# Performance work log

Hardware: AMD Instinct MI355X
Metric: run time of the kernel (lower is better)

## Reference

```python
import jax, jax.numpy as jnp
import numpy as np

NUM_EXPERTS = 4
TOP_K = 2


def setup_inputs() -> dict:
    key = jax.random.key(0)
    ks = jax.random.split(key, 16)
    B, L, D, E, H = 8, 768, 1024, NUM_EXPERTS, 4096
    s = 0.02
    return {
        "context_c": jax.random.normal(ks[0], (B, L, D), jnp.float32),
        "time_cond": jax.random.normal(ks[1], (B, D), jnp.float32),
        "gate_w": jax.random.normal(ks[2], (3 * D, E), jnp.float32) * s,
        "gate_b": jnp.zeros((E,), jnp.float32),
        "time_w": jax.random.normal(ks[3], (D, 2 * E), jnp.float32) * s,
        "time_b": jnp.zeros((2 * E,), jnp.float32),
        "ew1": jax.random.normal(ks[4], (E, D, H), jnp.float32) * s,
        "eb1": jnp.zeros((E, H), jnp.float32),
        "ew2": jax.random.normal(ks[5], (E, H, D), jnp.float32) * s,
        "eb2": jnp.zeros((E, D), jnp.float32),
        "sw1": jax.random.normal(ks[6], (D, H), jnp.float32) * s,
        "sb1": jnp.zeros((H,), jnp.float32),
        "sw2": jax.random.normal(ks[7], (H, D), jnp.float32) * s,
        "sb2": jnp.zeros((D,), jnp.float32),
    }


def reference(context_c, time_cond, gate_w, gate_b, time_w, time_b,
              ew1, eb1, ew2, eb2, sw1, sb1, sw2, sb2):
    B, L, D = context_c.shape
    E, K = NUM_EXPERTS, TOP_K
    L_head = L_wrist = L // 3

    head = context_c[:, :L_head]                       # (B, Lh, D)
    wrist = context_c[:, L_head:L_head + L_wrist]      # (B, Lw, D)
    proprio = context_c[:, L_head + L_wrist:]          # (B, Lp, D)

    # modality-combination aggregates for the gate
    full_agg = context_c.mean(axis=1)
    hp_agg = jnp.concatenate([head, proprio], axis=1).mean(axis=1)
    wp_agg = jnp.concatenate([wrist, proprio], axis=1).mean(axis=1)
    gate_in = jnp.concatenate([full_agg, hp_agg, wp_agg], axis=-1)  # (B, 3D)

    gate_logits = gate_in @ gate_w + gate_b            # (B, E)
    mod = jax.nn.silu(time_cond) @ time_w + time_b     # (B, 2E)
    scale, shift = jnp.split(mod, 2, axis=-1)
    gate_logits = gate_logits * (1.0 + scale) + shift

    gate_scores = jax.nn.softmax(gate_logits, axis=-1)
    topk_w, topk_i = jax.lax.top_k(gate_scores, K)     # (B, K)
    topk_w = topk_w / (topk_w.sum(axis=-1, keepdims=True) + 1e-8)

    # per-sample combine weight per expert: (B, E)
    onehot = (topk_i[..., None] == jnp.arange(E)[None, None, :]).astype(context_c.dtype)
    w_be = jnp.sum(topk_w[..., None] * onehot, axis=1)

    # modality token masks per expert: expert 1 skips wrist, expert 2 skips head
    mask = np.ones((E, L), dtype=np.float32)
    mask[1, L_head:L_head + L_wrist] = 0.0
    mask[2, :L_head] = 0.0
    mask = jnp.asarray(mask)

    out = jnp.zeros_like(context_c)
    for e in range(E):  # small fixed expert loop; FFN is tokenwise so masking == routing
        h = jax.nn.gelu(context_c @ ew1[e] + eb1[e], approximate=True)
        y = h @ ew2[e] + eb2[e]                        # (B, L, D)
        out = out + (w_be[:, e][:, None, None] * mask[e][None, :, None]) * y

    shared = jax.nn.gelu(context_c @ sw1 + sb1, approximate=True) @ sw2 + sb2
    return out + shared
```

## Files before the change

kernel.cpp:

```cpp
#include <hip/hip_runtime.h>

using bf16x8 = __attribute__((ext_vector_type(8))) short;
using f32x4  = __attribute__((ext_vector_type(4))) float;
using u16x4  = __attribute__((ext_vector_type(4))) unsigned short;

#define AS1(p) ((__attribute__((address_space(1))) void*)(p))
#define AS3(p) ((__attribute__((address_space(3))) void*)(p))

__device__ __forceinline__ unsigned short f2bf(float f){
  unsigned int x = __float_as_uint(f);
  unsigned int r = (x + 0x7FFFu + ((x >> 16) & 1u)) >> 16;
  return (unsigned short)r;
}
__device__ __forceinline__ float gelu_tanh(float x){
  float u = 0.7978845608028654f * (x + 0.044715f * x * x * x);
  float t = 1.f - 2.f / (__expf(2.f * u) + 1.f);
  return 0.5f * x * (1.f + t);
}

static constexpr int BB = 8, LL = 768, DD = 1024, HH = 4096, TT = 6144;

__global__ __launch_bounds__(256) void k0_transpose(const float* __restrict__ srcE,
                                                    const float* __restrict__ srcS,
                                                    unsigned short* __restrict__ dst,
                                                    int R, int C){
  __shared__ float tile[64][65];
  int z = blockIdx.z;
  const float* src = (z < 4) ? srcE + (size_t)z * R * C : srcS;
  unsigned short* d = dst + (size_t)z * R * C;
  int c0 = blockIdx.x * 64, r0 = blockIdx.y * 64;
  int tx = threadIdx.x & 15, ty = threadIdx.x >> 4;
  #pragma unroll
  for (int rep = 0; rep < 4; rep++){
    int r = ty + rep * 16;
    float4 v = *(const float4*)(src + (size_t)(r0 + r) * C + c0 + tx * 4);
    tile[r][tx * 4 + 0] = v.x; tile[r][tx * 4 + 1] = v.y;
    tile[r][tx * 4 + 2] = v.z; tile[r][tx * 4 + 3] = v.w;
  }
  __syncthreads();
  #pragma unroll
  for (int rep = 0; rep < 4; rep++){
    int c = ty + rep * 16;
    u16x4 o;
    o[0] = f2bf(tile[tx * 4 + 0][c]); o[1] = f2bf(tile[tx * 4 + 1][c]);
    o[2] = f2bf(tile[tx * 4 + 2][c]); o[3] = f2bf(tile[tx * 4 + 3][c]);
    *(u16x4*)(d + (size_t)(c0 + c) * R + r0 + tx * 4) = o;
  }
}

__global__ __launch_bounds__(256) void k1x_cvt_partial(const float* __restrict__ X,
                                                       unsigned short* __restrict__ Xb,
                                                       float* __restrict__ part){
  int ch = blockIdx.x, b = blockIdx.y, t = threadIdx.x;
  size_t rowbase = ((size_t)(b * LL + ch * 32)) * DD;
  const float4* src = (const float4*)(X + rowbase);
  u16x4* dst = (u16x4*)(Xb + rowbase);
  float4 s; s.x = s.y = s.z = s.w = 0.f;
  for (int l = 0; l < 32; l++){
    float4 v = src[l * 256 + t];
    u16x4 o;
    o[0] = f2bf(v.x); o[1] = f2bf(v.y); o[2] = f2bf(v.z); o[3] = f2bf(v.w);
    dst[l * 256 + t] = o;
    s.x += v.x; s.y += v.y; s.z += v.z; s.w += v.w;
  }
  ((float4*)(part + ((size_t)(b * 24 + ch)) * DD))[t] = s;
}

__global__ __launch_bounds__(256) void k1b_gate(const float* __restrict__ part,
                                                const float* __restrict__ tc,
                                                const float* __restrict__ gw,
                                                const float* __restrict__ gb,
                                                const float* __restrict__ tw,
                                                const float* __restrict__ tb,
                                                float* __restrict__ wtop, int* __restrict__ itop){
  int b = blockIdx.x, t = threadIdx.x;
  __shared__ float glog[4], gmod[8];
  if (t < 4) glog[t] = 0.f;
  if (t < 8) gmod[t] = 0.f;
  __syncthreads();
  float lacc[4] = {0.f,0.f,0.f,0.f};
  float macc[8] = {0.f,0.f,0.f,0.f,0.f,0.f,0.f,0.f};
  for (int dd = 0; dd < 4; dd++){
    int d = dd * 256 + t;
    const float* pb = part + (size_t)b * 24 * DD + d;
    float sh = 0.f, sw = 0.f, sp = 0.f;
    for (int c2 = 0; c2 < 8; c2++){
      sh += pb[(0  + c2) * DD];
      sw += pb[(8  + c2) * DD];
      sp += pb[(16 + c2) * DD];
    }
    float fa = (sh + sw + sp) * (1.f / 768.f);
    float hp = (sh + sp) * (1.f / 512.f);
    float wp = (sw + sp) * (1.f / 512.f);
    #pragma unroll
    for (int e = 0; e < 4; e++){
      lacc[e] += fa * gw[(size_t)d * 4 + e]
               + hp * gw[(size_t)(DD + d) * 4 + e]
               + wp * gw[(size_t)(2 * DD + d) * 4 + e];
    }
    float v = tc[(size_t)b * DD + d];
    float sl = v / (1.f + __expf(-v));
    #pragma unroll
    for (int j = 0; j < 8; j++) macc[j] += sl * tw[(size_t)d * 8 + j];
  }
  #pragma unroll
  for (int e = 0; e < 4; e++) atomicAdd(&glog[e], lacc[e]);
  #pragma unroll
  for (int j = 0; j < 8; j++) atomicAdd(&gmod[j], macc[j]);
  __syncthreads();
  if (t == 0){
    float lg[4];
    #pragma unroll
    for (int e = 0; e < 4; e++){
      float sc = gmod[e]     + tb[e];
      float sf = gmod[4 + e] + tb[4 + e];
      lg[e] = (glog[e] + gb[e]) * (1.f + sc) + sf;
    }
    float mx = fmaxf(fmaxf(lg[0], lg[1]), fmaxf(lg[2], lg[3]));
    float p[4], s = 0.f;
    #pragma unroll
    for (int e = 0; e < 4; e++){ p[e] = __expf(lg[e] - mx); s += p[e]; }
    #pragma unroll
    for (int e = 0; e < 4; e++) p[e] /= s;
    int i0 = 0;
    for (int e = 1; e < 4; e++) if (p[e] > p[i0]) i0 = e;
    int i1 = (i0 == 0) ? 1 : 0;
    for (int e = 0; e < 4; e++) if (e != i0 && p[e] > p[i1]) i1 = e;
    float den = p[i0] + p[i1] + 1e-8f;
    wtop[b * 2 + 0] = p[i0] / den;  wtop[b * 2 + 1] = p[i1] / den;
    itop[b * 2 + 0] = i0;           itop[b * 2 + 1] = i1;
  }
}

#define MMA_Q(AF, BQ, MH, NH)                                                   \
  {                                                                             \
    _Pragma("unroll") for (int ks = 0; ks < 2; ks++)                            \
    _Pragma("unroll") for (int mf = 0; mf < 4; mf++)                            \
    _Pragma("unroll") for (int nf = 0; nf < 2; nf++)                            \
      acc[(MH)*4+mf][(NH)*2+nf] = __builtin_amdgcn_mfma_f32_16x16x32_bf16(      \
          (AF)[mf][ks], (BQ)[nf][ks], acc[(MH)*4+mf][(NH)*2+nf], 0, 0, 0);      \
  }

__device__ __forceinline__ void gemm256_core(const unsigned short* __restrict__ A,
                                             const unsigned short* __restrict__ B,
                                             int lda, int ldb, int nkt,
                                             unsigned short* ldsA,
                                             unsigned short* ldsB,
                                             f32x4 (&acc)[8][4]){
  const int t = threadIdx.x;
  const int lane = t & 63, quad = lane >> 4, r = lane & 15;
  const int wave = t >> 6, wm = wave >> 2, wn = wave & 3;
  const int welem = (t & 448) * 8;

  int offA[2], offB[2];
  #pragma unroll
  for (int j = 0; j < 2; j++){
    int x = t * 16 + j * 8192;
    int y = x ^ (((x >> 7) & 7) << 4);
    int cr = y >> 7, kel = (y & 127) >> 1;
    offA[j] = (((cr >> 6) << 7) + (cr & 63)) * lda + kel;
    offB[j] = (((cr >> 5) << 6) + (cr & 31)) * ldb + kel;
  }
  const int ldam = 64 * lda, ldbn = 32 * ldb;

  auto stA = [&](int buf, int mh, int kt){
    #pragma unroll
    for (int j = 0; j < 2; j++)
      __builtin_amdgcn_global_load_lds(AS1(A + offA[j] + mh * ldam + kt * 64),
          AS3(ldsA + (buf * 2 + mh) * 8192 + welem + j * 4096), 16, 0, 0);
  };
  auto stB = [&](int buf, int nh, int kt){
    #pragma unroll
    for (int j = 0; j < 2; j++)
      __builtin_amdgcn_global_load_lds(AS1(B + offB[j] + nh * ldbn + kt * 64),
          AS3(ldsB + (buf * 2 + nh) * 8192 + welem + j * 4096), 16, 0, 0);
  };
  auto ldA = [&](int buf, int mh, bf16x8 (&dst)[4][2]){
    #pragma unroll
    for (int mf = 0; mf < 4; mf++){
      int cr = wm * 64 + mf * 16 + r;
      const unsigned short* p = ldsA + (buf * 2 + mh) * 8192 + cr * 64;
      int sw = (cr & 7) << 3;
      dst[mf][0] = *(const bf16x8*)(p + ((quad * 8) ^ sw));
      dst[mf][1] = *(const bf16x8*)(p + ((32 + quad * 8) ^ sw));
    }
  };
  auto ldB = [&](int buf, int nh, bf16x8 (&dst)[2][2]){
    #pragma unroll
    for (int nf = 0; nf < 2; nf++){
      int cc = wn * 32 + nf * 16 + r;
      const unsigned short* p = ldsB + (buf * 2 + nh) * 8192 + cc * 64;
      int sw = (cc & 7) << 3;
      dst[nf][0] = *(const bf16x8*)(p + ((quad * 8) ^ sw));
      dst[nf][1] = *(const bf16x8*)(p + ((32 + quad * 8) ^ sw));
    }
  };

  stA(0, 0, 0); stB(0, 0, 0); stB(0, 1, 0); stA(0, 1, 0);
  stA(1, 0, 1); stB(1, 0, 1); stB(1, 1, 1);
  asm volatile("s_waitcnt vmcnt(6)" ::: "memory");
  __builtin_amdgcn_s_barrier();

  bf16x8 af[4][2], b0[2][2], b1[2][2];
  for (int kt = 0; kt < nkt; kt++){
    int buf = kt & 1;
    bool pf1 = (kt + 1 < nkt), pf2 = (kt + 2 < nkt);
    ldA(buf, 0, af); ldB(buf, 0, b0);
    if (pf1) stA(buf ^ 1, 1, kt + 1);
    __builtin_amdgcn_s_barrier();
    __builtin_amdgcn_s_setprio(1);
    MMA_Q(af, b0, 0, 0);
    __builtin_amdgcn_s_setprio(0);
    __builtin_amdgcn_s_barrier();
    ldB(buf, 1, b1);
    if (pf2) stA(buf, 0, kt + 2);
    __builtin_amdgcn_s_barrier();
    __builtin_amdgcn_s_setprio(1);
    MMA_Q(af, b1, 0, 1);
    __builtin_amdgcn_s_setprio(0);
    __builtin_amdgcn_s_barrier();
    ldA(buf, 1, af);
    if (pf2) stB(buf, 0, kt + 2);
    __builtin_amdgcn_s_barrier();
    __builtin_amdgcn_s_setprio(1);
    MMA_Q(af, b1, 1, 1);
    __builtin_amdgcn_s_setprio(0);
    __builtin_amdgcn_s_barrier();
    if (pf2) stB(buf, 1, kt + 2);
    __builtin_amdgcn_s_barrier();
    __builtin_amdgcn_s_setprio(1);
    MMA_Q(af, b0, 1, 0);
    __builtin_amdgcn_s_setprio(0);
    if (pf1){
      if (pf2) asm volatile("s_waitcnt vmcnt(6)" ::: "memory");
      else     asm volatile("s_waitcnt vmcnt(0)" ::: "memory");
    }
    __builtin_amdgcn_s_barrier();
  }
}

__device__ __forceinline__ void mask_weight(int e, int seg, float& w){
  if ((e == 1 && seg == 1) || (e == 2 && seg == 0)) w = 0.f;
}

__global__ __launch_bounds__(512, 2) void k2_gemm1(const unsigned short* __restrict__ Xb,
                                                   const unsigned short* __restrict__ w1t,
                                                   const float* __restrict__ eb1,
                                                   const float* __restrict__ sb1,
                                                   const float* __restrict__ wtop,
                                                   const int* __restrict__ itop,
                                                   unsigned short* __restrict__ Hws){
  int m0 = blockIdx.x * 256, n0 = blockIdx.y * 256, slot = blockIdx.z;
  int b = m0 / LL, seg = (m0 % LL) / 256;
  int mat; float w;
  if (slot == 0){ mat = 4; w = 1.f; }
  else {
    int k = slot - 1;
    mat = itop[b * 2 + k];
    w = wtop[b * 2 + k];
    mask_weight(mat, seg, w);
    if (w == 0.f) return;
  }
  __shared__ __align__(16) unsigned short ldsA[32768];
  __shared__ __align__(16) unsigned short ldsB[32768];
  f32x4 acc[8][4];
  #pragma unroll
  for (int mi = 0; mi < 8; mi++)
    #pragma unroll
    for (int ni = 0; ni < 4; ni++)
      #pragma unroll
      for (int c = 0; c < 4; c++) acc[mi][ni][c] = 0.f;

  gemm256_core(Xb + (size_t)m0 * DD,
               w1t + (size_t)mat * HH * DD + (size_t)n0 * DD,
               DD, DD, DD / 64, ldsA, ldsB, acc);

  int t = threadIdx.x, lane = t & 63, wave = t >> 6;
  int quad = lane >> 4, r = lane & 15, wm = wave >> 2, wn = wave & 3;
  const float* b1 = (mat == 4) ? sb1 : eb1 + (size_t)mat * HH;
  unsigned short* Hout = Hws + (size_t)slot * TT * HH;
  #pragma unroll
  for (int ni = 0; ni < 4; ni++){
    int col = n0 + wn * 64 + ni * 16 + r;
    float bias = b1[col];
    #pragma unroll
    for (int mi = 0; mi < 8; mi++){
      #pragma unroll
      for (int r2 = 0; r2 < 4; r2++){
        int row = m0 + wm * 128 + mi * 16 + quad * 4 + r2;
        Hout[(size_t)row * HH + col] = f2bf(gelu_tanh(acc[mi][ni][r2] + bias) * w);
      }
    }
  }
}

__global__ __launch_bounds__(512, 2) void k3a_gemm2(const unsigned short* __restrict__ Hws,
                                                    const unsigned short* __restrict__ w2t,
                                                    const float* __restrict__ eb2,
                                                    const float* __restrict__ sb2,
                                                    const float* __restrict__ wtop,
                                                    const int* __restrict__ itop,
                                                    float* __restrict__ out,
                                                    float* __restrict__ p1){
  int m0 = blockIdx.x * 256, n0 = blockIdx.y * 256, kh = blockIdx.z;
  int b = m0 / LL, seg = (m0 % LL) / 256;
  __shared__ __align__(16) unsigned short ldsA[32768];
  __shared__ __align__(16) unsigned short ldsB[32768];
  f32x4 acc[8][4];
  #pragma unroll
  for (int mi = 0; mi < 8; mi++)
    #pragma unroll
    for (int ni = 0; ni < 4; ni++)
      #pragma unroll
      for (int c = 0; c < 4; c++) acc[mi][ni][c] = 0.f;

  int emat[2]; float ew[2];
  #pragma unroll
  for (int k = 0; k < 2; k++){
    emat[k] = itop[b * 2 + k];
    ew[k] = wtop[b * 2 + k];
    mask_weight(emat[k], seg, ew[k]);
  }
  for (int slot = 0; slot < 3; slot++){
    int mat;
    if (slot == 0) mat = 4;
    else { if (ew[slot - 1] == 0.f) continue; mat = emat[slot - 1]; }
    gemm256_core(Hws + (size_t)slot * TT * HH + (size_t)m0 * HH + kh * 2048,
                 w2t + (size_t)mat * DD * HH + (size_t)n0 * HH + kh * 2048,
                 HH, HH, 2048 / 64, ldsA, ldsB, acc);
  }
  int t = threadIdx.x, lane = t & 63, wave = t >> 6;
  int quad = lane >> 4, r = lane & 15, wm = wave >> 2, wn = wave & 3;
  if (kh == 0){
    #pragma unroll
    for (int ni = 0; ni < 4; ni++){
      int col = n0 + wn * 64 + ni * 16 + r;
      float bias = sb2[col];
      if (ew[0] > 0.f) bias += ew[0] * eb2[(size_t)emat[0] * DD + col];
      if (ew[1] > 0.f) bias += ew[1] * eb2[(size_t)emat[1] * DD + col];
      #pragma unroll
      for (int mi = 0; mi < 8; mi++)
        #pragma unroll
        for (int r2 = 0; r2 < 4; r2++){
          int row = m0 + wm * 128 + mi * 16 + quad * 4 + r2;
          out[(size_t)row * DD + col] = acc[mi][ni][r2] + bias;
        }
    }
  } else {
    #pragma unroll
    for (int ni = 0; ni < 4; ni++){
      int col = n0 + wn * 64 + ni * 16 + r;
      #pragma unroll
      for (int mi = 0; mi < 8; mi++)
        #pragma unroll
        for (int r2 = 0; r2 < 4; r2++){
          int row = m0 + wm * 128 + mi * 16 + quad * 4 + r2;
          p1[(size_t)row * DD + col] = acc[mi][ni][r2];
        }
    }
  }
}

__global__ __launch_bounds__(256) void k3r_reduce(float* __restrict__ out,
                                                  const float* __restrict__ p1){
  size_t i = (size_t)blockIdx.x * 256 + threadIdx.x;
  float4 a = ((const float4*)out)[i];
  float4 b = ((const float4*)p1)[i];
  a.x += b.x; a.y += b.y; a.z += b.z; a.w += b.w;
  ((float4*)out)[i] = a;
}

extern "C" void kernel_launch(void* const* d_in, const int* in_sizes, int n_in,
                              void* d_out, int out_size, void* d_ws, size_t ws_size,
                              hipStream_t stream){
  const float* X   = (const float*)d_in[0];
  const float* tc  = (const float*)d_in[1];
  const float* gw  = (const float*)d_in[2];
  const float* gb  = (const float*)d_in[3];
  const float* tw  = (const float*)d_in[4];
  const float* tb  = (const float*)d_in[5];
  const float* ew1 = (const float*)d_in[6];
  const float* eb1 = (const float*)d_in[7];
  const float* ew2 = (const float*)d_in[8];
  const float* eb2 = (const float*)d_in[9];
  const float* sw1 = (const float*)d_in[10];
  const float* sb1 = (const float*)d_in[11];
  const float* sw2 = (const float*)d_in[12];
  const float* sb2 = (const float*)d_in[13];
  float* out = (float*)d_out;
  char* ws = (char*)d_ws;

  const size_t off_part = 0;
  const size_t off_wtop = 786432;
  const size_t off_itop = 786560;
  const size_t off_xb   = 1ull << 20;
  const size_t off_w1t  = 14ull << 20;
  const size_t off_w2t  = off_w1t + 41943040ull;
  const size_t off_h    = off_w2t + 41943040ull;
  const size_t need     = off_h + 150994944ull;
  if (ws_size < need) return;

  float* part = (float*)(ws + off_part);
  float* wtop = (float*)(ws + off_wtop);
  int*   itop = (int*)(ws + off_itop);
  unsigned short* Xb  = (unsigned short*)(ws + off_xb);
  unsigned short* w1t = (unsigned short*)(ws + off_w1t);
  unsigned short* w2t = (unsigned short*)(ws + off_w2t);
  unsigned short* Hws = (unsigned short*)(ws + off_h);
  float* p1 = (float*)(ws + off_w1t);

  k1x_cvt_partial<<<dim3(24, 8), 256, 0, stream>>>(X, Xb, part);
  k0_transpose<<<dim3(64, 16, 5), 256, 0, stream>>>(ew1, sw1, w1t, 1024, 4096);
  k0_transpose<<<dim3(16, 64, 5), 256, 0, stream>>>(ew2, sw2, w2t, 4096, 1024);
  k1b_gate<<<dim3(8), 256, 0, stream>>>(part, tc, gw, gb, tw, tb, wtop, itop);
  k2_gemm1<<<dim3(24, 16, 3), 512, 0, stream>>>(Xb, w1t, eb1, sb1, wtop, itop, Hws);
  k3a_gemm2<<<dim3(24, 4, 2), 512, 0, stream>>>(Hws, w2t, eb2, sb2, wtop, itop, out, p1);
  k3r_reduce<<<dim3(6144), 256, 0, stream>>>(out, p1);
}
```

Baseline: 634.5 us.

## Unroll k-loop by two with compile-time buffers and add XCD-aware block swizzle

The GEMM main loop is unrolled by two so the LDS double-buffer index becomes a compile-time constant, and the last two iterations are peeled, which removes runtime buffer arithmetic and prefetch predicates from the steady state. Both GEMM kernels also remap their linear block index so that consecutive logical tiles land on the same XCD, aiming for better L2 reuse of shared A and B tiles. The remap assumes the total block count divides evenly by 8 and that nkt is at least 2. The unrolled loop may raise code size and register pressure.

```diff
diff --git a/kernel.cpp b/kernel.cpp
--- a/kernel.cpp
+++ b/kernel.cpp
@@ -6,6 +6,8 @@
 
 #define AS1(p) ((__attribute__((address_space(1))) void*)(p))
 #define AS3(p) ((__attribute__((address_space(3))) void*)(p))
+
+template<int V> struct Ic { static constexpr int value = V; };
 
 __device__ __forceinline__ unsigned short f2bf(float f){
   unsigned int x = __float_as_uint(f);
@@ -196,37 +198,31 @@
     }
   };
 
-  stA(0, 0, 0); stB(0, 0, 0); stB(0, 1, 0); stA(0, 1, 0);
-  stA(1, 0, 1); stB(1, 0, 1); stB(1, 1, 1);
-  asm volatile("s_waitcnt vmcnt(6)" ::: "memory");
-  __builtin_amdgcn_s_barrier();
-
-  bf16x8 af[4][2], b0[2][2], b1[2][2];
-  for (int kt = 0; kt < nkt; kt++){
-    int buf = kt & 1;
-    bool pf1 = (kt + 1 < nkt), pf2 = (kt + 2 < nkt);
-    ldA(buf, 0, af); ldB(buf, 0, b0);
-    if (pf1) stA(buf ^ 1, 1, kt + 1);
+  auto ktile = [&](auto bufc, int kt, bool pf1, bool pf2){
+    constexpr int BUF = decltype(bufc)::value;
+    bf16x8 af[4][2], b0[2][2], b1[2][2];
+    ldA(BUF, 0, af); ldB(BUF, 0, b0);
+    if (pf1) stA(BUF ^ 1, 1, kt + 1);
     __builtin_amdgcn_s_barrier();
     __builtin_amdgcn_s_setprio(1);
     MMA_Q(af, b0, 0, 0);
     __builtin_amdgcn_s_setprio(0);
     __builtin_amdgcn_s_barrier();
-    ldB(buf, 1, b1);
-    if (pf2) stA(buf, 0, kt + 2);
+    ldB(BUF, 1, b1);
+    if (pf2) stA(BUF, 0, kt + 2);
     __builtin_amdgcn_s_barrier();
     __builtin_amdgcn_s_setprio(1);
     MMA_Q(af, b1, 0, 1);
     __builtin_amdgcn_s_setprio(0);
     __builtin_amdgcn_s_barrier();
-    ldA(buf, 1, af);
-    if (pf2) stB(buf, 0, kt + 2);
+    ldA(BUF, 1, af);
+    if (pf2) stB(BUF, 0, kt + 2);
     __builtin_amdgcn_s_barrier();
     __builtin_amdgcn_s_setprio(1);
     MMA_Q(af, b1, 1, 1);
     __builtin_amdgcn_s_setprio(0);
     __builtin_amdgcn_s_barrier();
-    if (pf2) stB(buf, 1, kt + 2);
+    if (pf2) stB(BUF, 1, kt + 2);
     __builtin_amdgcn_s_barrier();
     __builtin_amdgcn_s_setprio(1);
     MMA_Q(af, b0, 1, 0);
@@ -236,11 +232,33 @@
       else     asm volatile("s_waitcnt vmcnt(0)" ::: "memory");
     }
     __builtin_amdgcn_s_barrier();
-  }
+  };
+
+  stA(0, 0, 0); stB(0, 0, 0); stB(0, 1, 0); stA(0, 1, 0);
+  stA(1, 0, 1); stB(1, 0, 1); stB(1, 1, 1);
+  asm volatile("s_waitcnt vmcnt(6)" ::: "memory");
+  __builtin_amdgcn_s_barrier();
+
+  int kt = 0;
+  for (; kt + 2 < nkt; kt += 2){
+    ktile(Ic<0>{}, kt,     true, true);
+    ktile(Ic<1>{}, kt + 1, true, true);
+  }
+  ktile(Ic<0>{}, nkt - 2, true,  false);
+  ktile(Ic<1>{}, nkt - 1, false, false);
 }
 
 __device__ __forceinline__ void mask_weight(int e, int seg, float& w){
   if ((e == 1 && seg == 1) || (e == 2 && seg == 0)) w = 0.f;
+}
+
+template<int GX, int GY>
+__device__ __forceinline__ void xcd_swizzle(int& bx, int& by, int& bz){
+  int lin = blockIdx.x + GX * (blockIdx.y + GY * blockIdx.z);
+  int nwg = GX * GY * gridDim.z;
+  int q = nwg >> 3;
+  int swz = (lin & 7) * q + (lin >> 3);
+  bx = swz % GX; int rem = swz / GX; by = rem % GY; bz = rem / GY;
 }
 
 __global__ __launch_bounds__(512, 2) void k2_gemm1(const unsigned short* __restrict__ Xb,
@@ -250,7 +268,8 @@
                                                    const float* __restrict__ wtop,
                                                    const int* __restrict__ itop,
                                                    unsigned short* __restrict__ Hws){
-  int m0 = blockIdx.x * 256, n0 = blockIdx.y * 256, slot = blockIdx.z;
+  int bx, by, bz; xcd_swizzle<24, 16>(bx, by, bz);
+  int m0 = bx * 256, n0 = by * 256, slot = bz;
   int b = m0 / LL, seg = (m0 % LL) / 256;
   int mat; float w;
   if (slot == 0){ mat = 4; w = 1.f; }
@@ -302,7 +321,8 @@
                                                     const int* __restrict__ itop,
                                                     float* __restrict__ out,
                                                     float* __restrict__ p1){
-  int m0 = blockIdx.x * 256, n0 = blockIdx.y * 256, kh = blockIdx.z;
+  int bx, by, bz; xcd_swizzle<24, 4>(bx, by, bz);
+  int m0 = bx * 256, n0 = by * 256, kh = bz;
   int b = m0 / LL, seg = (m0 % LL) / 256;
   __shared__ __align__(16) unsigned short ldsA[32768];
   __shared__ __align__(16) unsigned short ldsB[32768];
```

After: 643.2 us. Within noise of the previous version (+1.4%).
